# Kernel optimization log

Hardware: AMD Instinct MI355X
Metric: run time of the kernel (lower is better)

Reference implementation:

```python
import jax, jax.numpy as jnp
import numpy as np

B, L, D_MODEL = 2, 4096, 1024
D_INNER = 2048  # expand * d_model
D_CONV = 4


def setup_inputs() -> dict:
    key = jax.random.key(0)
    ks = jax.random.split(key, 7)
    return {
        "hidden_states": jax.random.normal(ks[0], (B, L, D_MODEL), jnp.float32),
        "W_in": jax.random.normal(ks[1], (2 * D_INNER, D_MODEL), jnp.float32) * 0.02,
        "conv_w": jax.random.normal(ks[2], (D_INNER, D_CONV), jnp.float32) * 0.1,
        "conv_b": jax.random.normal(ks[3], (D_INNER,), jnp.float32) * 0.1,
        "k_ssm": jax.random.normal(ks[4], (D_INNER, L), jnp.float32) * 0.02,  # materialized SSM kernel (channels=1)
        "D_skip": jax.random.normal(ks[5], (D_INNER,), jnp.float32),
        "W_out": jax.random.normal(ks[6], (D_MODEL, D_INNER), jnp.float32) * 0.02,
    }


def _silu(x):
    return x * jax.nn.sigmoid(x)


def reference(hidden_states, W_in, conv_w, conv_b, k_ssm, D_skip, W_out):
    Bq, Lq, _ = hidden_states.shape
    # in_proj (no bias): (B, L, d_model) -> (B, 2*d_inner, L)
    xz = jnp.einsum('bld,ed->bel', hidden_states, W_in)
    x, z = jnp.split(xz, 2, axis=1)  # each (B, d_inner, L)

    # causal depthwise conv1d (pad left d_conv-1) + SiLU (causal_conv1d_fn)
    xp = jnp.pad(x, ((0, 0), (0, 0), (D_CONV - 1, 0)))
    xc = conv_b[None, :, None]
    for j in range(D_CONV):
        xc = xc + conv_w[None, :, j, None] * xp[:, :, j:j + Lq]
    x = _silu(xc)

    # FFT long convolution (l_kernel = L, n = 2L), channels = 1
    n = 2 * Lq
    x_f = jnp.fft.rfft(x, n=n)            # (B, H, n//2+1) complex
    k_f = jnp.fft.rfft(k_ssm, n=n)        # (H, n//2+1)
    y = jnp.fft.irfft(x_f * k_f[None], n=n)[..., :Lq]  # (B, H, L)

    # D skip connection
    y = y + x * D_skip[None, :, None]

    # gating with SiLU(z)
    y = y * _silu(z)

    # out_proj (no bias): (B, H, L) -> (B, L, d_model)
    return jnp.einsum('bhl,dh->bld', y, W_out)
```

## Files before the change

kernel.cpp:

```cpp
#include <hip/hip_runtime.h>
#include <hip/hip_bf16.h>
#include <math.h>

#define B_SZ 2
#define L_SZ 4096
#define DM   1024
#define DI   2048
#define E_SZ 4096
#define DC   4

typedef unsigned short u16;
typedef __attribute__((ext_vector_type(8))) short short8;
typedef __attribute__((ext_vector_type(4))) float f32x4;

__device__ __forceinline__ float silu_f(float v) {
    return v / (1.0f + __expf(-v));
}

__device__ __forceinline__ void split_bf16(float x, u16& h, u16& l) {
    unsigned u  = __float_as_uint(x);
    unsigned hb = u & 0xFFFF0000u;
    h = (u16)(hb >> 16);
    float lf = x - __uint_as_float(hb);
    l = (u16)(__float_as_uint(lf) >> 16);
}
__device__ __forceinline__ float bf2f(u16 h) {
    return __uint_as_float(((unsigned)h) << 16);
}

__device__ __forceinline__ void gld_lds16(const u16* g, u16* l) {
    __builtin_amdgcn_global_load_lds(
        (const __attribute__((address_space(1))) unsigned int*)g,
        (__attribute__((address_space(3))) unsigned int*)l, 16, 0, 0);
}

__device__ __forceinline__ void mfma_triple(
    f32x4& acc, short8 ah, short8 al, short8 bh, short8 bl)
{
    acc = __builtin_amdgcn_mfma_f32_16x16x32_bf16(ah, bh, acc, 0, 0, 0);
    acc = __builtin_amdgcn_mfma_f32_16x16x32_bf16(ah, bl, acc, 0, 0, 0);
    acc = __builtin_amdgcn_mfma_f32_16x16x32_bf16(al, bh, acc, 0, 0, 0);
}

__device__ __forceinline__ void kperm(const unsigned* cur, short8& ah, short8& al) {
    union { unsigned u[4]; short8 s; } A_, B_;
    #pragma unroll
    for (int i = 0; i < 4; ++i) {
        A_.u[i] = __builtin_amdgcn_perm(cur[2*i+1], cur[2*i], 0x05040100u);
        B_.u[i] = __builtin_amdgcn_perm(cur[2*i+1], cur[2*i], 0x07060302u);
    }
    ah = A_.s; al = B_.s;
}
__device__ __forceinline__ void kpref(const unsigned* kp, int c1, unsigned* nxt) {
    #pragma unroll
    for (int e = 0; e < 8; ++e) nxt[e] = kp[32*c1 - e];
}

__global__ __launch_bounds__(256) void pack_rm(
    const float* __restrict__ X, u16* __restrict__ H, u16* __restrict__ Lo,
    int ldx, int r16n, long sX, long sOut)
{
    const long cid = (long)blockIdx.x * 256 + threadIdx.x;
    const int  qc  = (int)(cid & 63);
    const long blk = cid >> 6;
    const int  r16 = (int)(blk % r16n);
    const int  k32 = (int)(blk / r16n);
    const int  q = qc >> 4, m = qc & 15;

    const float* src = X + blockIdx.y * sX + (long)(r16 * 16 + m) * ldx + k32 * 32 + q * 8;
    float4 v0 = *(const float4*)src;
    float4 v1 = *(const float4*)(src + 4);
    float v[8] = {v0.x,v0.y,v0.z,v0.w,v1.x,v1.y,v1.z,v1.w};

    u16 hs[8], ls[8];
    #pragma unroll
    for (int j = 0; j < 8; ++j) split_bf16(v[j], hs[j], ls[j]);

    const long o = blockIdx.y * sOut + cid * 8;
    *(uint4*)&H[o]  = *(const uint4*)hs;
    *(uint4*)&Lo[o] = *(const uint4*)ls;
}

__global__ __launch_bounds__(256) void gemm_mfma(
    const u16* __restrict__ Ah, const u16* __restrict__ Al,
    const u16* __restrict__ Bh, const u16* __restrict__ Bl,
    float* __restrict__ C,
    int r16A, int r16B, long sA, long sB, long sC,
    int ldc, int nk32)
{
    __shared__ alignas(16) u16 sm[4][4096];

    const int tid  = threadIdx.x;
    const int wv   = tid >> 6, lane = tid & 63;
    const long zb  = blockIdx.z;

    const int nbx = gridDim.x;
    const int nwg = gridDim.x * gridDim.y;
    int flat = blockIdx.x + nbx * blockIdx.y;
    const int cpx = nwg >> 3;
    flat = (flat & 7) * cpx + (flat >> 3);
    const int bx = flat % nbx, by = flat / nbx;

    const u16* srcs0 = Ah + zb * sA;
    const u16* srcs1 = Al + zb * sA;
    const u16* srcs2 = Bh + zb * sB;
    const u16* srcs3 = Bl + zb * sB;
    const u16* mysrc = (wv == 0) ? srcs0 : (wv == 1) ? srcs1 : (wv == 2) ? srcs2 : srcs3;
    const int  rblk  = (wv < 2) ? bx * 8 : by * 8;
    const int  r16c  = (wv < 2) ? r16A : r16B;
    u16* myl = sm[wv];

    const int wr = wv >> 1, wc = wv & 1;

    f32x4 acc[4][4];
    #pragma unroll
    for (int i = 0; i < 4; ++i)
        #pragma unroll
        for (int j = 0; j < 4; ++j)
            #pragma unroll
            for (int r = 0; r < 4; ++r) acc[i][j][r] = 0.f;

    for (int s = 0; s < nk32; ++s) {
        if (s) __syncthreads();
        {
            const u16* g = mysrc + (((long)s * r16c + rblk) << 9) + lane * 8;
            #pragma unroll
            for (int i = 0; i < 8; ++i)
                gld_lds16(g + (i << 9), myl + (i << 9));
        }
        __syncthreads();

        short8 afh[4], afl[4], bfh[4], bfl[4];
        const int aoff = (wr * 4) * 512 + lane * 8;
        const int boff = (wc * 4) * 512 + lane * 8;
        #pragma unroll
        for (int t = 0; t < 4; ++t) {
            afh[t] = *(const short8*)&sm[0][aoff + t * 512];
            afl[t] = *(const short8*)&sm[1][aoff + t * 512];
            bfh[t] = *(const short8*)&sm[2][boff + t * 512];
            bfl[t] = *(const short8*)&sm[3][boff + t * 512];
        }
        #pragma unroll
        for (int i = 0; i < 4; ++i)
            #pragma unroll
            for (int j = 0; j < 4; ++j) {
                acc[i][j] = __builtin_amdgcn_mfma_f32_16x16x32_bf16(afh[i], bfh[j], acc[i][j], 0, 0, 0);
                acc[i][j] = __builtin_amdgcn_mfma_f32_16x16x32_bf16(afh[i], bfl[j], acc[i][j], 0, 0, 0);
                acc[i][j] = __builtin_amdgcn_mfma_f32_16x16x32_bf16(afl[i], bfh[j], acc[i][j], 0, 0, 0);
            }
    }

    const int m_ = lane & 15, q_ = lane >> 4;
    float* Cb = C + zb * sC;
    const int row00 = bx * 128 + wr * 64 + q_ * 4;
    const int col0  = by * 128 + wc * 64 + m_;
    #pragma unroll
    for (int i = 0; i < 4; ++i)
        #pragma unroll
        for (int j = 0; j < 4; ++j) {
            const long base = (long)(row00 + i * 16) * ldc + col0 + j * 16;
            #pragma unroll
            for (int r = 0; r < 4; ++r)
                Cb[base + (long)r * ldc] = acc[i][j][r];
        }
}

__global__ __launch_bounds__(256) void conv_silu_split(
    const float* __restrict__ xz, const float* __restrict__ conv_w,
    const float* __restrict__ conv_b,
    u16* __restrict__ xh_gl, u16* __restrict__ xl_gl)
{
    const long gid = (long)blockIdx.x * 256 + threadIdx.x;
    const int  q   = (int)(gid % (L_SZ / 4));
    const long bc  = gid / (L_SZ / 4);
    const int  ch  = (int)(bc % DI);
    const int  b   = (int)(bc / DI);

    const float* row = xz + ((long)b * E_SZ + ch) * L_SZ;
    const int l0 = q * 4;

    float4 cur  = *(const float4*)&row[l0];
    float4 prev = q ? *(const float4*)&row[l0 - 4] : make_float4(0.f, 0.f, 0.f, 0.f);

    const float w0 = conv_w[ch*DC+0], w1 = conv_w[ch*DC+1];
    const float w2 = conv_w[ch*DC+2], w3 = conv_w[ch*DC+3];
    const float bias = conv_b[ch];

    float o[4];
    o[0] = silu_f(bias + w0*prev.y + w1*prev.z + w2*prev.w + w3*cur.x);
    o[1] = silu_f(bias + w0*prev.z + w1*prev.w + w2*cur.x  + w3*cur.y);
    o[2] = silu_f(bias + w0*prev.w + w1*cur.x  + w2*cur.y  + w3*cur.z);
    o[3] = silu_f(bias + w0*cur.x  + w1*cur.y  + w2*cur.z  + w3*cur.w);

    unsigned long long hp = 0ull, lp = 0ull;
    #pragma unroll
    for (int r = 0; r < 4; ++r) {
        u16 h, l; split_bf16(o[r], h, l);
        hp |= ((unsigned long long)h) << (16*r);
        lp |= ((unsigned long long)l) << (16*r);
    }
    const long base = ((long)b * DI + ch) * L_SZ + l0;
    *(unsigned long long*)&xh_gl[base] = hp;
    *(unsigned long long*)&xl_gl[base] = lp;
}

__global__ __launch_bounds__(256) void pack_k(
    const float* __restrict__ k_ssm, unsigned* __restrict__ kv)
{
    const long gid = (long)blockIdx.x * 256 + threadIdx.x;
    const int  qq  = (int)(gid & (L_SZ / 4 - 1));
    const int  ch  = (int)(gid >> 10);

    const long off = ((long)ch << 12) + qq * 4;
    float4 v = *(const float4*)&k_ssm[off];
    float f[4] = { v.x, v.y, v.z, v.w };
    unsigned o[4];
    #pragma unroll
    for (int r = 0; r < 4; ++r) {
        u16 h, l; split_bf16(f[r], h, l);
        o[r] = (unsigned)h | ((unsigned)l << 16);
    }
    *(uint4*)&kv[off] = *(const uint4*)o;
}

__global__ __launch_bounds__(256, 6) void longconv_mfma(
    u16* __restrict__ xh_gl, u16* __restrict__ xl_gl,
    const float* __restrict__ xz,  const unsigned* __restrict__ kv,
    const float* __restrict__ D_skip)
{
    __shared__ alignas(16) u16 XH[4352];
    __shared__ alignas(16) u16 XL[4352];

    const int tid  = threadIdx.x;
    const int lane = tid & 63;
    const int wv   = tid >> 6;
    const int wc   = blockIdx.x;
    const int ch   = wc & (DI - 1);
    const int b    = wc >> 11;

    u16*            xhr = xh_gl + ((long)b * DI + ch) * L_SZ;
    u16*            xlr = xl_gl + ((long)b * DI + ch) * L_SZ;
    const unsigned* kvr = kv + ((long)ch << 12);

    if (tid < 64) {
        uint4 z = make_uint4(0u, 0u, 0u, 0u);
        ((uint4*)((tid < 32) ? XH : XL))[tid & 31] = z;
    }
    {
        const int ck = wv * 2;
        gld_lds16(xhr + (ck    ) * 512 + lane * 8, XH + 256 + (ck    ) * 512);
        gld_lds16(xhr + (ck + 1) * 512 + lane * 8, XH + 256 + (ck + 1) * 512);
        gld_lds16(xlr + (ck    ) * 512 + lane * 8, XL + 256 + (ck    ) * 512);
        gld_lds16(xlr + (ck + 1) * 512 + lane * 8, XL + 256 + (ck + 1) * 512);
    }
    __syncthreads();

    const int m_ = lane & 15;
    const int q_ = lane >> 4;
    const int dq = m_ - 8 * q_ + ((q_ >= 2) ? 32 : 0);
    const int xoff_lane = 256 + 16 * m_ + 8 * q_ - ((q_ >= 2) ? 32 : 0);

    const int tset[4] = { wv, 7 - wv, 8 + wv, 15 - wv };
    const int tmax = 15 - wv;
    const int cmax = 8 * tmax + 7;

    f32x4 acc[4];
    #pragma unroll
    for (int u = 0; u < 4; ++u)
        #pragma unroll
        for (int r = 0; r < 4; ++r) acc[u][r] = 0.f;

    const unsigned* kp = kvr + dq;

    unsigned lcur[8];
    #pragma unroll
    for (int e = 0; e < 8; ++e) {
        const int ki = dq - e;
        lcur[e] = (ki >= 0) ? kvr[ki] : 0u;
    }

    for (int c = 0; c <= cmax; ++c) {
        short8 ah, al;
        kperm(lcur, ah, al);

        unsigned lnext[8];
        if (c < cmax) kpref(kp, c + 1, lnext);

        const int xbase = xoff_lane - 32 * c;
        #pragma unroll
        for (int u = 0; u < 4; ++u) {
            const int t = tset[u];
            if (8 * t >= c - 7) {
                short8 bh = *(const short8*)&XH[xbase + 256 * t];
                short8 bl = *(const short8*)&XL[xbase + 256 * t];
                acc[u] = __builtin_amdgcn_mfma_f32_16x16x32_bf16(ah, bh, acc[u], 0, 0, 0);
                acc[u] = __builtin_amdgcn_mfma_f32_16x16x32_bf16(ah, bl, acc[u], 0, 0, 0);
                acc[u] = __builtin_amdgcn_mfma_f32_16x16x32_bf16(al, bh, acc[u], 0, 0, 0);
            }
        }

        if (c < cmax) {
            #pragma unroll
            for (int e = 0; e < 8; ++e) lcur[e] = lnext[e];
        }
    }

    const float  Ds   = D_skip[ch];
    const float* zrow = xz + ((long)b * E_SZ + DI + ch) * L_SZ;

    #pragma unroll
    for (int u = 0; u < 4; ++u) {
        const int t  = tset[u];
        const int l0 = 256 * t + 16 * m_ + 4 * q_;
        float4 zv = *(const float4*)&zrow[l0];
        float zt[4] = { zv.x, zv.y, zv.z, zv.w };
        unsigned long long hp = 0ull, lp = 0ull;
        #pragma unroll
        for (int r = 0; r < 4; ++r) {
            const float xf = bf2f(XH[256 + l0 + r]) + bf2f(XL[256 + l0 + r]);
            const float o  = (acc[u][r] + Ds * xf) * silu_f(zt[r]);
            u16 h, l; split_bf16(o, h, l);
            hp |= ((unsigned long long)h) << (16*r);
            lp |= ((unsigned long long)l) << (16*r);
        }
        *(unsigned long long*)&xhr[l0] = hp;
        *(unsigned long long*)&xlr[l0] = lp;
    }
}

__global__ __launch_bounds__(256) void pack_y(
    const u16* __restrict__ Yh, const u16* __restrict__ Yl,
    u16* __restrict__ OH, u16* __restrict__ OL, long sOut)
{
    __shared__ u16 T[2][32][136];
    const int t  = threadIdx.x;
    const int l0 = blockIdx.x * 128;
    const int h0 = blockIdx.y * 32;
    const int b  = blockIdx.z;

    const u16* yb_h = Yh + ((long)b * DI + h0) * L_SZ + l0;
    const u16* yb_l = Yl + ((long)b * DI + h0) * L_SZ + l0;

    #pragma unroll
    for (int i = 0; i < 2; ++i) {
        const int c = t + 256 * i;
        const int row = c >> 4, col = (c & 15) * 8;
        *(uint4*)&T[0][row][col] = *(const uint4*)&yb_h[(long)row * L_SZ + col];
        *(uint4*)&T[1][row][col] = *(const uint4*)&yb_l[(long)row * L_SZ + col];
    }
    __syncthreads();

    u16* outs[2] = { OH + b * sOut, OL + b * sOut };
    #pragma unroll
    for (int p = 0; p < 2; ++p) {
        #pragma unroll
        for (int i = 0; i < 2; ++i) {
            const int c = t + 256 * i;
            const int r16b = c >> 6, qc = c & 63;
            const int q = qc >> 4, m = qc & 15;
            const int l = r16b * 16 + m;
            u16 vals[8];
            #pragma unroll
            for (int j = 0; j < 8; ++j) vals[j] = T[p][q * 8 + j][l];
            const long o = ((long)(blockIdx.y * 256 + blockIdx.x * 8 + r16b) << 9) + qc * 8;
            *(uint4*)&outs[p][o] = *(const uint4*)vals;
        }
    }
}

extern "C" void kernel_launch(void* const* d_in, const int* in_sizes, int n_in,
                              void* d_out, int out_size, void* d_ws, size_t ws_size,
                              hipStream_t stream)
{
    const float* hidden = (const float*)d_in[0];
    const float* W_in   = (const float*)d_in[1];
    const float* conv_w = (const float*)d_in[2];
    const float* conv_b = (const float*)d_in[3];
    const float* k_ssm  = (const float*)d_in[4];
    const float* D_skip = (const float*)d_in[5];
    const float* W_out  = (const float*)d_in[6];
    float* out = (float*)d_out;

    char* ws = (char*)d_ws;
    float* xz  = (float*)ws;
    u16*   xh  = (u16*)(ws + 134217728);
    u16*   xl  = (u16*)(ws + 167772160);
    u16*   WinH  = (u16*)(ws + 201326592);
    u16*   WinL  = WinH + 4194304;
    u16*   WoutH = (u16*)(ws + 201326592);
    u16*   WoutL = WoutH + 2097152;
    u16*   hidH  = (u16*)(ws + 218103808);
    u16*   hidL  = hidH + 8388608;
    unsigned* klv = (unsigned*)ws;
    u16*   yAh   = (u16*)ws;
    u16*   yAl   = yAh + 8388608;

    pack_rm<<<dim3(2048, 1), 256, 0, stream>>>(W_in, WinH, WinL, DM, 256, 0L, 0L);
    pack_rm<<<dim3(2048, B_SZ), 256, 0, stream>>>(hidden, hidH, hidL, DM, 256,
        (long)L_SZ * DM, 4194304L);

    gemm_mfma<<<dim3(32, 32, B_SZ), 256, 0, stream>>>(
        WinH, WinL, hidH, hidL, xz,
        256, 256, 0L, 4194304L, (long)E_SZ * L_SZ, L_SZ, 32);

    conv_silu_split<<<dim3((unsigned)((long)B_SZ*DI*(L_SZ/4)/256)), 256, 0, stream>>>(
        xz, conv_w, conv_b, xh, xl);

    pack_k<<<dim3((unsigned)((long)DI * (L_SZ/4) / 256)), 256, 0, stream>>>(k_ssm, klv);

    longconv_mfma<<<dim3(B_SZ * DI), 256, 0, stream>>>(
        xh, xl, xz, klv, D_skip);

    pack_rm<<<dim3(1024, 1), 256, 0, stream>>>(W_out, WoutH, WoutL, DI, 64, 0L, 0L);

    pack_y<<<dim3(32, 64, B_SZ), 256, 0, stream>>>(
        xh, xl, yAh, yAl, 33554432L);

    gemm_mfma<<<dim3(32, 8, B_SZ), 256, 0, stream>>>(
        yAh, yAl, WoutH, WoutL, out,
        256, 64, 33554432L, 0L, (long)L_SZ * DM, DM, 64);
}
```

Before: 654.3 us.

## Use 256x256 double-buffered GEMM kernel for the input projection

Adds a new 512-thread GEMM kernel with 256x256 output tiles, double-buffered LDS staging that prefetches the next K-slice while computing the current one, and s_setprio around the MFMA bursts. The in_proj GEMM now launches this kernel instead of the 128x128 one. The aim is more operand reuse per LDS load and overlap of global loads with compute. The original kernel also loses its XCD-aware block swizzle, which may change L2 locality for the out_proj GEMM that still uses it. The larger tile launches only 512 blocks, and launch bounds of one block per SM limit occupancy.

```diff
diff --git a/kernel.cpp b/kernel.cpp
--- a/kernel.cpp
+++ b/kernel.cpp
@@ -94,19 +94,12 @@
     const int wv   = tid >> 6, lane = tid & 63;
     const long zb  = blockIdx.z;
 
-    const int nbx = gridDim.x;
-    const int nwg = gridDim.x * gridDim.y;
-    int flat = blockIdx.x + nbx * blockIdx.y;
-    const int cpx = nwg >> 3;
-    flat = (flat & 7) * cpx + (flat >> 3);
-    const int bx = flat % nbx, by = flat / nbx;
-
     const u16* srcs0 = Ah + zb * sA;
     const u16* srcs1 = Al + zb * sA;
     const u16* srcs2 = Bh + zb * sB;
     const u16* srcs3 = Bl + zb * sB;
     const u16* mysrc = (wv == 0) ? srcs0 : (wv == 1) ? srcs1 : (wv == 2) ? srcs2 : srcs3;
-    const int  rblk  = (wv < 2) ? bx * 8 : by * 8;
+    const int  rblk  = (wv < 2) ? blockIdx.x * 8 : blockIdx.y * 8;
     const int  r16c  = (wv < 2) ? r16A : r16B;
     u16* myl = sm[wv];
 
@@ -152,10 +145,117 @@
 
     const int m_ = lane & 15, q_ = lane >> 4;
     float* Cb = C + zb * sC;
-    const int row00 = bx * 128 + wr * 64 + q_ * 4;
-    const int col0  = by * 128 + wc * 64 + m_;
+    const int row00 = blockIdx.x * 128 + wr * 64 + q_ * 4;
+    const int col0  = blockIdx.y * 128 + wc * 64 + m_;
     #pragma unroll
     for (int i = 0; i < 4; ++i)
+        #pragma unroll
+        for (int j = 0; j < 4; ++j) {
+            const long base = (long)(row00 + i * 16) * ldc + col0 + j * 16;
+            #pragma unroll
+            for (int r = 0; r < 4; ++r)
+                Cb[base + (long)r * ldc] = acc[i][j][r];
+        }
+}
+
+__global__ __launch_bounds__(512, 1) void gemm256(
+    const u16* __restrict__ Ah, const u16* __restrict__ Al,
+    const u16* __restrict__ Bh, const u16* __restrict__ Bl,
+    float* __restrict__ C,
+    int r16A, int r16B, long sA, long sB, long sC,
+    int ldc, int nk32)
+{
+    __shared__ alignas(16) u16 sm[2][64][512];
+
+    const int tid  = threadIdx.x;
+    const int wv   = tid >> 6, lane = tid & 63;
+    const long zb  = blockIdx.z;
+    const int bx = blockIdx.x, by = blockIdx.y;
+
+    const int wr  = wv >> 2;
+    const int wcn = wv & 3;
+
+    const u16* planes0 = Ah + zb * sA;
+    const u16* planes1 = Al + zb * sA;
+    const u16* planes2 = Bh + zb * sB;
+    const u16* planes3 = Bl + zb * sB;
+    const int  pidx  = wv >> 1;
+    const u16* psrc  = (pidx == 0) ? planes0 : (pidx == 1) ? planes1
+                     : (pidx == 2) ? planes2 : planes3;
+    const int  rbase = ((pidx < 2) ? bx : by) * 16 + (wv & 1) * 8;
+    const int  r16n  = (pidx < 2) ? r16A : r16B;
+    const int  dblk  = (pidx << 4) + ((wv & 1) << 3);
+
+    auto STAGE = [&](int buf, int s) {
+        const u16* g = psrc + (((long)s * r16n + rbase) << 9) + lane * 8;
+        u16* d = &sm[buf][dblk][0] + lane * 8;
+        #pragma unroll
+        for (int i = 0; i < 8; ++i)
+            gld_lds16(g + (i << 9), d + (i << 9));
+    };
+
+    f32x4 acc[8][4];
+    #pragma unroll
+    for (int i = 0; i < 8; ++i)
+        #pragma unroll
+        for (int j = 0; j < 4; ++j)
+            #pragma unroll
+            for (int r = 0; r < 4; ++r) acc[i][j][r] = 0.f;
+
+    STAGE(0, 0);
+    int cur = 0;
+    const int lo = lane * 8;
+
+    for (int s = 0; s < nk32; ++s) {
+        __syncthreads();
+        if (s + 1 < nk32) STAGE(cur ^ 1, s + 1);
+
+        short8 bfh[4], bfl[4];
+        #pragma unroll
+        for (int j = 0; j < 4; ++j) {
+            bfh[j] = *(const short8*)&sm[cur][32 + wcn * 4 + j][lo];
+            bfl[j] = *(const short8*)&sm[cur][48 + wcn * 4 + j][lo];
+        }
+
+        {
+            short8 afh[4], afl[4];
+            #pragma unroll
+            for (int i = 0; i < 4; ++i) {
+                afh[i] = *(const short8*)&sm[cur][     wr * 8 + i][lo];
+                afl[i] = *(const short8*)&sm[cur][16 + wr * 8 + i][lo];
+            }
+            __builtin_amdgcn_s_setprio(1);
+            #pragma unroll
+            for (int i = 0; i < 4; ++i)
+                #pragma unroll
+                for (int j = 0; j < 4; ++j)
+                    mfma_triple(acc[i][j], afh[i], afl[i], bfh[j], bfl[j]);
+            __builtin_amdgcn_s_setprio(0);
+        }
+        {
+            short8 afh[4], afl[4];
+            #pragma unroll
+            for (int i = 0; i < 4; ++i) {
+                afh[i] = *(const short8*)&sm[cur][     wr * 8 + 4 + i][lo];
+                afl[i] = *(const short8*)&sm[cur][16 + wr * 8 + 4 + i][lo];
+            }
+            __builtin_amdgcn_s_setprio(1);
+            #pragma unroll
+            for (int i = 0; i < 4; ++i)
+                #pragma unroll
+                for (int j = 0; j < 4; ++j)
+                    mfma_triple(acc[4 + i][j], afh[i], afl[i], bfh[j], bfl[j]);
+            __builtin_amdgcn_s_setprio(0);
+        }
+        cur ^= 1;
+    }
+
+    const int m_ = lane & 15, q_ = lane >> 4;
+    float* Cb = C + zb * sC;
+    const int row00 = bx * 256 + wr * 128 + q_ * 4;
+    const int col0  = by * 256 + wcn * 64 + m_;
+    #pragma unroll
+    for (int i = 0; i < 8; ++i)
         #pragma unroll
         for (int j = 0; j < 4; ++j) {
             const long base = (long)(row00 + i * 16) * ldc + col0 + j * 16;
@@ -399,7 +499,7 @@
     pack_rm<<<dim3(2048, B_SZ), 256, 0, stream>>>(hidden, hidH, hidL, DM, 256,
         (long)L_SZ * DM, 4194304L);
 
-    gemm_mfma<<<dim3(32, 32, B_SZ), 256, 0, stream>>>(
+    gemm256<<<dim3(16, 16, B_SZ), 512, 0, stream>>>(
         WinH, WinL, hidH, hidL, xz,
         256, 256, 0L, 4194304L, (long)E_SZ * L_SZ, L_SZ, 32);
 
```

Result: faster. 625.8 us (-4.4%).
